# Kernel optimization log

Measured on AMD Instinct MI355X. Metric: run time of the kernel, lower is better.

Reference implementation:

```python
import jax, jax.numpy as jnp
import numpy as np

H = 64          # rnn_hidden_dim
HYP = 64        # api_hyper_dim
N_AG = 8
N_EN = 8
N_AL = 7
E_FEAT = 9
A_FEAT = 10
OWN_FEAT = 16
N_ACT = 14


def setup_inputs() -> dict:
    key = jax.random.key(0)
    ks = jax.random.split(key, 24)
    bs = 4096
    inp = {
        "own_feats": jax.random.normal(ks[0], (bs * N_AG, OWN_FEAT), jnp.float32),
        "enemy_feats": jax.random.normal(ks[1], (bs * N_AG * N_EN, E_FEAT), jnp.float32),
        "ally_feats": jax.random.normal(ks[2], (bs * N_AG * N_AL, A_FEAT), jnp.float32),
        "hidden_state": jax.random.normal(ks[3], (bs * N_AG, H), jnp.float32),
        "agent_indices": jax.random.randint(ks[4], (bs * N_AG,), 0, N_AG),
        "last_action_indices": jax.random.randint(ks[5], (bs * N_AG,), 0, N_ACT),
        "bs": bs,
    }
    s = 0.05
    inp.update({
        "fc1_own_w": jax.random.normal(ks[6], (OWN_FEAT, H), jnp.float32) * s,
        "fc1_own_b": jnp.zeros((H,), jnp.float32),
        "agent_id_emb": jax.random.normal(ks[7], (N_AG, H), jnp.float32) * s,
        "action_id_emb": jax.random.normal(ks[8], (N_ACT, H), jnp.float32) * s,
        "he_w1": jax.random.normal(ks[9], (E_FEAT, HYP), jnp.float32) * s,
        "he_b1": jnp.zeros((HYP,), jnp.float32),
        "he_w2": jax.random.normal(ks[10], (HYP, (E_FEAT + 1) * H + 1), jnp.float32) * s,
        "he_b2": jnp.zeros(((E_FEAT + 1) * H + 1,), jnp.float32),
        "ha_w1": jax.random.normal(ks[11], (A_FEAT, HYP), jnp.float32) * s,
        "ha_b1": jnp.zeros((HYP,), jnp.float32),
        "ha_w2": jax.random.normal(ks[12], (HYP, A_FEAT * H), jnp.float32) * s,
        "ha_b2": jnp.zeros((A_FEAT * H,), jnp.float32),
        "gru_w_ih": jax.random.normal(ks[13], (3 * H, H), jnp.float32) * s,
        "gru_w_hh": jax.random.normal(ks[14], (3 * H, H), jnp.float32) * s,
        "gru_b_ih": jnp.zeros((3 * H,), jnp.float32),
        "gru_b_hh": jnp.zeros((3 * H,), jnp.float32),
        "fc2_w": jax.random.normal(ks[15], (H, 6), jnp.float32) * s,
        "fc2_b": jnp.zeros((6,), jnp.float32),
    })
    return inp


def reference(own_feats, enemy_feats, ally_feats, hidden_state,
              fc1_own_w, fc1_own_b, agent_id_emb, action_id_emb,
              he_w1, he_b1, he_w2, he_b2, ha_w1, ha_b1, ha_w2, ha_b2,
              gru_w_ih, gru_w_hh, gru_b_ih, gru_b_hh, fc2_w, fc2_b,
              agent_indices, last_action_indices, bs):
    # own embedding + id/action embeddings  [bs*n_ag, H]
    emb_own = own_feats @ fc1_own_w + fc1_own_b
    emb_own = emb_own + agent_id_emb[agent_indices] + action_id_emb[last_action_indices]

    # enemy hypernet: [bs*n_ag*n_en, (E_FEAT+1)*H + 1]
    hyper_e = jax.nn.relu(enemy_feats @ he_w1 + he_b1) @ he_w2 + he_b2
    fc1_w_e = hyper_e[:, :-(H + 1)].reshape(-1, E_FEAT, H)
    emb_en = jnp.einsum('ne,neh->nh', enemy_feats, fc1_w_e)
    emb_en = emb_en.reshape(bs * N_AG, N_EN, H).sum(axis=1)

    # ally hypernet (non-MMM): [bs*n_ag*n_al, A_FEAT*H]
    hyper_a = jax.nn.relu(ally_feats @ ha_w1 + ha_b1) @ ha_w2 + ha_b2
    fc1_w_a = hyper_a.reshape(-1, A_FEAT, H)
    emb_al = jnp.einsum('na,nah->nh', ally_feats, fc1_w_a)
    emb_al = emb_al.reshape(bs * N_AG, N_AL, H).sum(axis=1)

    x = jax.nn.relu(emb_own + emb_en + emb_al)

    # torch GRUCell
    h_in = hidden_state.reshape(-1, H)
    gi = x @ gru_w_ih.T + gru_b_ih
    gh = h_in @ gru_w_hh.T + gru_b_hh
    i_r, i_z, i_n = jnp.split(gi, 3, axis=-1)
    h_r, h_z, h_n = jnp.split(gh, 3, axis=-1)
    r = jax.nn.sigmoid(i_r + h_r)
    z = jax.nn.sigmoid(i_z + h_z)
    n = jnp.tanh(i_n + r * h_n)
    hh = (1.0 - z) * n + z * h_in

    q_normal = (hh @ fc2_w + fc2_b).reshape(bs, N_AG, 6)

    # attack head from enemy hypernet tail
    fc2_w_attack = hyper_e[:, -(H + 1):-1].reshape(bs * N_AG, N_EN, H)
    fc2_b_attack = hyper_e[:, -1].reshape(bs * N_AG, N_EN)
    q_attack = (jnp.einsum('nh,neh->ne', hh, fc2_w_attack) + fc2_b_attack).reshape(bs, N_AG, N_EN)

    q = jnp.concatenate([q_normal, q_attack], axis=-1)
    return q.reshape(bs, N_AG, -1), hh.reshape(bs, N_AG, H)
```

## Files before the change

kernel.cpp:

```cpp
#include <hip/hip_runtime.h>
#include <hip/hip_bf16.h>

typedef short short8 __attribute__((ext_vector_type(8)));
typedef float f32x4 __attribute__((ext_vector_type(4)));

#define HD 64
#define N_EN 8
#define N_AL 7
#define E_FEAT 9
#define A_FEAT 10
#define OWN_FEAT 16
#define N_ACT 14
#define EW2 641
#define AW2 640

#define KSE 20
#define KSA 21
#define KSG 5
#define KSU 3

#define BE_OFF 0
#define BE_CNT (KSE*4*64*8)
#define BA_OFF (BE_OFF+BE_CNT)
#define BA_CNT (KSA*4*64*8)
#define BG_OFF (BA_OFF+BA_CNT)
#define BG_CNT (KSG*16*64*8)
#define BU_OFF (BG_OFF+BG_CNT)
#define BU_CNT (KSU*5*64*8)
#define WS_SHORTS (BU_OFF+BU_CNT)

#define P_STRIDE 676
#define LDS_AG 0
#define LDS_GATES 8192
#define LDS_AU 17024
#define LDS_U 0
#define LDS_BYTES 21632

__device__ __forceinline__ ushort f2u(float x) {
    __hip_bfloat16 b = __float2bfloat16(x);
    ushort u; __builtin_memcpy(&u, &b, 2); return u;
}
__device__ __forceinline__ float u2f(uint u) {
    union { uint x; float f; } c; c.x = u << 16; return c.f;
}
__device__ __forceinline__ uint pk2(float a, float b) {
    return (uint)f2u(a) | ((uint)f2u(b) << 16);
}
__device__ __forceinline__ float sigm(float x) { return 1.f / (1.f + __expf(-x)); }
__device__ __forceinline__ short8 lda(const char* base, int row, int strideB, int s, int g) {
    const char* p = base + row * strideB + s * 64 + g * 8;
    union { short8 v; uint2 q[2]; } u;
    u.q[0] = *(const uint2*)p;
    u.q[1] = *(const uint2*)(p + 32);
    return u.v;
}

__global__ __launch_bounds__(256) void prep_kernel(
    const float* __restrict__ he_w2, const float* __restrict__ he_b2,
    const float* __restrict__ ha_w2, const float* __restrict__ ha_b2,
    const float* __restrict__ fc1_own_w, const float* __restrict__ fc1_own_b,
    const float* __restrict__ agent_id_emb, const float* __restrict__ action_id_emb,
    const float* __restrict__ gru_w_ih, const float* __restrict__ gru_w_hh,
    const float* __restrict__ gru_b_ih, const float* __restrict__ gru_b_hh,
    const float* __restrict__ fc2_w, const float* __restrict__ fc2_b,
    ushort* __restrict__ ws)
{
    const int GE = KSE * 4, GA = KSA * 4, GG = KSG * 16, GU = KSU * 5;
    const int total = (GE + GA + GG + GU) * 64;
    int idx = blockIdx.x * 256 + threadIdx.x;
    if (idx >= total) return;
    int grp = idx >> 6, lane = idx & 63;
    int g = lane >> 4, col16 = lane & 15;
    int table, s, t, slot;
    if (grp < GE)           { table = 0; int q = grp;            s = q / 4;  t = q % 4;  slot = q * 64 + lane; }
    else if (grp < GE + GA) { table = 1; int q = grp - GE;       s = q / 4;  t = q % 4;  slot = q * 64 + lane; }
    else if (grp < GE + GA + GG) { table = 2; int q = grp - GE - GA; s = q / 16; t = q % 16; slot = q * 64 + lane; }
    else                    { table = 3; int q = grp - GE - GA - GG; s = q / 5; t = q % 5; slot = q * 64 + lane; }
    const int j = t * 16 + col16;
    ushort out[8];
    #pragma unroll
    for (int e = 0; e < 8; ++e) {
        int kk = 32 * s + 4 * g + (e & 3) + 16 * (e >> 2);
        float v = 0.f;
        if (table == 0) {
            if (kk < 576)      { int f = kk >> 6, k = kk & 63; v = he_w2[k * EW2 + f * HD + j]; }
            else if (kk < 585) { int f = kk - 576; v = he_b2[f * HD + j]; }
            else if (kk < 601) { int f = kk - 585; v = fc1_own_w[f * HD + j]; }
            else if (kk == 601){ v = fc1_own_b[j]; }
            else if (kk < 610) { int a = kk - 602; v = agent_id_emb[a * HD + j]; }
            else if (kk < 624) { int a = kk - 610; v = action_id_emb[a * HD + j]; }
        } else if (table == 1) {
            if (kk < 640)      { int f = kk >> 6, k = kk & 63; v = ha_w2[k * AW2 + f * HD + j]; }
            else if (kk < 650) { int f = kk - 640; v = ha_b2[f * HD + j]; }
        } else if (table == 2) {
            int gb = j >> 6, c = j & 63;
            if (gb <= 1) {
                int jj = gb * 64 + c;
                if (kk < 64)        v = gru_w_ih[jj * HD + kk];
                else if (kk < 128)  v = gru_w_hh[jj * HD + kk - 64];
                else if (kk == 128) v = gru_b_ih[jj] + gru_b_hh[jj];
            } else if (gb == 2) {
                int jj = 128 + c;
                if (kk < 64)        v = gru_w_ih[jj * HD + kk];
                else if (kk == 128) v = gru_b_ih[jj];
            } else {
                int jj = 128 + c;
                if (kk >= 64 && kk < 128) v = gru_w_hh[jj * HD + kk - 64];
                else if (kk == 128)       v = gru_b_hh[jj];
            }
        } else {
            if (j < 64) {
                if (kk < 64)       v = he_w2[j * EW2 + 576 + kk];
                else if (kk == 64) v = he_w2[j * EW2 + 640];
            } else if (j < 70) {
                int o = j - 64;
                if (kk < 64)       v = fc2_w[kk * 6 + o];
                else if (kk == 64) v = fc2_b[o];
            } else if (j == 70) {
                if (kk < 64)       v = he_b2[576 + kk];
                else if (kk == 64) v = he_b2[640];
            }
        }
        out[e] = f2u(v);
    }
    ushort* dst = ws + ((table == 0) ? BE_OFF : (table == 1) ? BA_OFF : (table == 2) ? BG_OFF : BU_OFF);
    *(short8*)(dst + slot * 8) = *(short8*)out;
}

__global__ __launch_bounds__(256, 2) void agent_kernel(
    const float* __restrict__ own_feats,
    const float* __restrict__ enemy_feats,
    const float* __restrict__ ally_feats,
    const float* __restrict__ hidden_state,
    const int*  __restrict__ agent_idx,
    const int*  __restrict__ last_act_idx,
    const float* __restrict__ he_w1, const float* __restrict__ he_b1,
    const float* __restrict__ ha_w1, const float* __restrict__ ha_b1,
    const ushort* __restrict__ ws,
    float* __restrict__ out_q, float* __restrict__ out_hh)
{
    __shared__ __align__(16) char smem[LDS_BYTES];
    const int tid  = threadIdx.x;
    const int lane = tid & 63;
    const int wv   = tid >> 6;
    const int n0   = blockIdx.x * 16;
    const int arow = lane & 15;
    const int g    = lane >> 4;
    ushort* P = (ushort*)smem;

    {
        float w1[E_FEAT];
        #pragma unroll
        for (int f = 0; f < E_FEAT; ++f) w1[f] = he_w1[f * HD + lane];
        const float b1 = he_b1[lane];
        #pragma unroll
        for (int rr = 0; rr < 4; ++rr) {
            const int row = wv * 4 + rr, n = n0 + row;
            const float* efb = enemy_feats + (size_t)n * (N_EN * E_FEAT);
            float pf[E_FEAT], sf[E_FEAT];
            #pragma unroll
            for (int f = 0; f < E_FEAT; ++f) { pf[f] = 0.f; sf[f] = 0.f; }
            #pragma unroll
            for (int e = 0; e < N_EN; ++e) {
                float ef[E_FEAT];
                #pragma unroll
                for (int f = 0; f < E_FEAT; ++f) ef[f] = efb[e * E_FEAT + f];
                float acc = b1;
                #pragma unroll
                for (int f = 0; f < E_FEAT; ++f) acc += ef[f] * w1[f];
                const float r = fmaxf(acc, 0.f);
                #pragma unroll
                for (int f = 0; f < E_FEAT; ++f) { pf[f] += r * ef[f]; sf[f] += ef[f]; }
            }
            ushort* Pr = P + row * P_STRIDE;
            #pragma unroll
            for (int f = 0; f < E_FEAT; ++f) Pr[f * HD + lane] = f2u(pf[f]);
            if (lane == 0) {
                #pragma unroll
                for (int f = 0; f < E_FEAT; ++f) Pr[576 + f] = f2u(sf[f]);
                Pr[601] = 0x3F80;
            }
            if (lane < OWN_FEAT) Pr[585 + lane] = f2u(own_feats[(size_t)n * OWN_FEAT + lane]);
            const int ai = agent_idx[n], la = last_act_idx[n];
            if (lane < 8)      Pr[602 + lane] = (lane == ai) ? 0x3F80 : 0;
            if (lane < N_ACT)  Pr[610 + lane] = (lane == la) ? 0x3F80 : 0;
            if (lane < 16)     Pr[624 + lane] = 0;
        }
    }
    __syncthreads();

    f32x4 accE = {0.f, 0.f, 0.f, 0.f};
    #pragma unroll
    for (int s = 0; s < KSE; ++s) {
        short8 b = *(const short8*)(ws + BE_OFF + ((size_t)(s * 4 + wv) * 64 + lane) * 8);
        short8 a = lda(smem, arow, P_STRIDE * 2, s, g);
        accE = __builtin_amdgcn_mfma_f32_16x16x32_bf16(a, b, accE, 0, 0, 0);
    }
    __syncthreads();

    {
        float w1[A_FEAT];
        #pragma unroll
        for (int f = 0; f < A_FEAT; ++f) w1[f] = ha_w1[f * HD + lane];
        const float b1 = ha_b1[lane];
        #pragma unroll
        for (int rr = 0; rr < 4; ++rr) {
            const int row = wv * 4 + rr, n = n0 + row;
            const float* afb = ally_feats + (size_t)n * (N_AL * A_FEAT);
            float pf[A_FEAT], sf[A_FEAT];
            #pragma unroll
            for (int f = 0; f < A_FEAT; ++f) { pf[f] = 0.f; sf[f] = 0.f; }
            #pragma unroll
            for (int e = 0; e < N_AL; ++e) {
                float af[A_FEAT];
                #pragma unroll
                for (int f = 0; f < A_FEAT; ++f) af[f] = afb[e * A_FEAT + f];
                float acc = b1;
                #pragma unroll
                for (int f = 0; f < A_FEAT; ++f) acc += af[f] * w1[f];
                const float r = fmaxf(acc, 0.f);
                #pragma unroll
                for (int f = 0; f < A_FEAT; ++f) { pf[f] += r * af[f]; sf[f] += af[f]; }
            }
            ushort* Pr = P + row * P_STRIDE;
            #pragma unroll
            for (int f = 0; f < A_FEAT; ++f) Pr[f * HD + lane] = f2u(pf[f]);
            if (lane == 0) {
                #pragma unroll
                for (int f = 0; f < A_FEAT; ++f) Pr[640 + f] = f2u(sf[f]);
            }
            if (lane < 22) Pr[650 + lane] = 0;
        }
    }
    __syncthreads();

    #pragma unroll
    for (int s = 0; s < KSA; ++s) {
        short8 b = *(const short8*)(ws + BA_OFF + ((size_t)(s * 4 + wv) * 64 + lane) * 8);
        short8 a = lda(smem, arow, P_STRIDE * 2, s, g);
        accE = __builtin_amdgcn_mfma_f32_16x16x32_bf16(a, b, accE, 0, 0, 0);
    }
    __syncthreads();

    float4 h4s;
    #pragma unroll
    for (int j = 0; j < 4; ++j) {
        const int m = g * 4 + j;
        *(ushort*)(smem + LDS_AG + m * 328 + (wv * 16 + arow) * 2) = f2u(fmaxf(accE[j], 0.f));
    }
    {
        const int row = tid >> 4, c4 = (tid & 15) * 4;
        h4s = *(const float4*)(hidden_state + (size_t)(n0 + row) * HD + c4);
        char* p = smem + LDS_AG + row * 328 + (64 + c4) * 2;
        *(uint*)p       = pk2(h4s.x, h4s.y);
        *(uint*)(p + 4) = pk2(h4s.z, h4s.w);
        if (tid < 16) *(ushort*)(smem + LDS_AG + tid * 328 + 128 * 2) = 0x3F80;
        for (int i = tid; i < 16 * 31; i += 256) {
            int r2 = i / 31, c = 129 + i % 31;
            *(ushort*)(smem + LDS_AG + r2 * 328 + c * 2) = 0;
        }
    }
    __syncthreads();

    {
        f32x4 accG[4] = {{0.f,0.f,0.f,0.f},{0.f,0.f,0.f,0.f},{0.f,0.f,0.f,0.f},{0.f,0.f,0.f,0.f}};
        #pragma unroll
        for (int s = 0; s < KSG; ++s) {
            short8 a = lda(smem + LDS_AG, arow, 328, s, g);
            #pragma unroll
            for (int tt = 0; tt < 4; ++tt) {
                const int t = wv * 4 + tt;
                short8 b = *(const short8*)(ws + BG_OFF + ((size_t)(s * 16 + t) * 64 + lane) * 8);
                accG[tt] = __builtin_amdgcn_mfma_f32_16x16x32_bf16(a, b, accG[tt], 0, 0, 0);
            }
        }
        #pragma unroll
        for (int tt = 0; tt < 4; ++tt)
            #pragma unroll
            for (int j = 0; j < 4; ++j) {
                const int m = g * 4 + j, jc = (wv * 4 + tt) * 16 + arow;
                *(ushort*)(smem + LDS_GATES + m * 520 + jc * 2) = f2u(accG[tt][j]);
            }
    }
    __syncthreads();

    {
        const int row = tid >> 4, c4 = (tid & 15) * 4;
        const char* gb = smem + LDS_GATES + row * 520;
        uint2 rv = *(const uint2*)(gb + c4 * 2);
        uint2 zv = *(const uint2*)(gb + 128 + c4 * 2);
        uint2 iv = *(const uint2*)(gb + 256 + c4 * 2);
        uint2 nv = *(const uint2*)(gb + 384 + c4 * 2);
        float hr[4] = {u2f(rv.x & 0xffffu), u2f(rv.x >> 16), u2f(rv.y & 0xffffu), u2f(rv.y >> 16)};
        float hz[4] = {u2f(zv.x & 0xffffu), u2f(zv.x >> 16), u2f(zv.y & 0xffffu), u2f(zv.y >> 16)};
        float hi[4] = {u2f(iv.x & 0xffffu), u2f(iv.x >> 16), u2f(iv.y & 0xffffu), u2f(iv.y >> 16)};
        float hn[4] = {u2f(nv.x & 0xffffu), u2f(nv.x >> 16), u2f(nv.y & 0xffffu), u2f(nv.y >> 16)};
        float hcur[4] = {h4s.x, h4s.y, h4s.z, h4s.w};
        float hh[4];
        #pragma unroll
        for (int cc = 0; cc < 4; ++cc) {
            const float r = sigm(hr[cc]);
            const float z = sigm(hz[cc]);
            const float nng = tanhf(hi[cc] + r * hn[cc]);
            hh[cc] = (1.f - z) * nng + z * hcur[cc];
        }
        *(float4*)(out_hh + (size_t)(n0 + row) * HD + c4) = make_float4(hh[0], hh[1], hh[2], hh[3]);
        char* p = smem + LDS_AU + row * 200 + c4 * 2;
        *(uint*)p       = pk2(hh[0], hh[1]);
        *(uint*)(p + 4) = pk2(hh[2], hh[3]);
        if (tid < 16) *(ushort*)(smem + LDS_AU + tid * 200 + 64 * 2) = 0x3F80;
        for (int i = tid; i < 16 * 31; i += 256) {
            int r2 = i / 31, c = 65 + i % 31;
            *(ushort*)(smem + LDS_AU + r2 * 200 + c * 2) = 0;
        }
    }
    __syncthreads();

    {
        f32x4 accU = {0.f, 0.f, 0.f, 0.f};
        f32x4 accQ = {0.f, 0.f, 0.f, 0.f};
        #pragma unroll
        for (int s = 0; s < KSU; ++s) {
            short8 a = lda(smem + LDS_AU, arow, 200, s, g);
            short8 b = *(const short8*)(ws + BU_OFF + ((size_t)(s * 5 + wv) * 64 + lane) * 8);
            accU = __builtin_amdgcn_mfma_f32_16x16x32_bf16(a, b, accU, 0, 0, 0);
            if (wv == 0) {
                short8 b2 = *(const short8*)(ws + BU_OFF + ((size_t)(s * 5 + 4) * 64 + lane) * 8);
                accQ = __builtin_amdgcn_mfma_f32_16x16x32_bf16(a, b2, accQ, 0, 0, 0);
            }
        }
        float* uld = (float*)(smem + LDS_U);
        #pragma unroll
        for (int j = 0; j < 4; ++j) {
            const int m = g * 4 + j;
            uld[m * 66 + wv * 16 + arow] = accU[j];
        }
        if (wv == 0) {
            #pragma unroll
            for (int j = 0; j < 4; ++j) {
                const int m = g * 4 + j;
                if (arow < 6)       out_q[(size_t)(n0 + m) * N_ACT + arow] = accQ[j];
                else if (arow == 6) uld[m * 66 + 64] = accQ[j];
            }
        }
    }
    __syncthreads();

    {
        float w1[E_FEAT];
        #pragma unroll
        for (int f = 0; f < E_FEAT; ++f) w1[f] = he_w1[f * HD + lane];
        const float b1 = he_b1[lane];
        const float* uld = (const float*)(smem + LDS_U);
        #pragma unroll
        for (int rr = 0; rr < 4; ++rr) {
            const int row = wv * 4 + rr, n = n0 + row;
            const float uk = uld[row * 66 + lane];
            const float ct = uld[row * 66 + 64];
            const float* efb = enemy_feats + (size_t)n * (N_EN * E_FEAT);
            float p[N_EN];
            #pragma unroll
            for (int e = 0; e < N_EN; ++e) {
                float acc = b1;
                #pragma unroll
                for (int f = 0; f < E_FEAT; ++f) acc += efb[e * E_FEAT + f] * w1[f];
                p[e] = fmaxf(acc, 0.f) * uk;
            }
            #pragma unroll
            for (int o = 1; o < 64; o <<= 1) {
                #pragma unroll
                for (int e = 0; e < N_EN; ++e) p[e] += __shfl_xor(p[e], o);
            }
            if (lane < N_EN) {
                float pv = p[0];
                #pragma unroll
                for (int e = 1; e < N_EN; ++e) if (lane == e) pv = p[e];
                out_q[(size_t)n * N_ACT + 6 + lane] = pv + ct;
            }
        }
    }
}

extern "C" void kernel_launch(void* const* d_in, const int* in_sizes, int n_in,
                              void* d_out, int out_size, void* d_ws, size_t ws_size,
                              hipStream_t stream) {
    const float* own_feats    = (const float*)d_in[0];
    const float* enemy_feats  = (const float*)d_in[1];
    const float* ally_feats   = (const float*)d_in[2];
    const float* hidden_state = (const float*)d_in[3];
    const int*  agent_idx     = (const int*)d_in[4];
    const int*  last_act      = (const int*)d_in[5];
    const float* fc1_own_w = (const float*)d_in[7];
    const float* fc1_own_b = (const float*)d_in[8];
    const float* agent_id_emb  = (const float*)d_in[9];
    const float* action_id_emb = (const float*)d_in[10];
    const float* he_w1 = (const float*)d_in[11];
    const float* he_b1 = (const float*)d_in[12];
    const float* he_w2 = (const float*)d_in[13];
    const float* he_b2 = (const float*)d_in[14];
    const float* ha_w1 = (const float*)d_in[15];
    const float* ha_b1 = (const float*)d_in[16];
    const float* ha_w2 = (const float*)d_in[17];
    const float* ha_b2 = (const float*)d_in[18];
    const float* gru_w_ih = (const float*)d_in[19];
    const float* gru_w_hh = (const float*)d_in[20];
    const float* gru_b_ih = (const float*)d_in[21];
    const float* gru_b_hh = (const float*)d_in[22];
    const float* fc2_w = (const float*)d_in[23];
    const float* fc2_b = (const float*)d_in[24];

    const int R = in_sizes[0] / OWN_FEAT;
    ushort* ws = (ushort*)d_ws;
    float* out_q  = (float*)d_out;
    float* out_hh = out_q + (size_t)R * N_ACT;

    prep_kernel<<<65, 256, 0, stream>>>(
        he_w2, he_b2, ha_w2, ha_b2, fc1_own_w, fc1_own_b,
        agent_id_emb, action_id_emb, gru_w_ih, gru_w_hh, gru_b_ih, gru_b_hh,
        fc2_w, fc2_b, ws);

    agent_kernel<<<R / 16, 256, 0, stream>>>(
        own_feats, enemy_feats, ally_feats, hidden_state, agent_idx, last_act,
        he_w1, he_b1, ha_w1, ha_b1, ws, out_q, out_hh);
}
```

Measured before the change: 111.0 us.

## Double-buffer two 16-row tiles per block to overlap P-building with MFMA

```diff
diff --git a/kernel.cpp b/kernel.cpp
--- a/kernel.cpp
+++ b/kernel.cpp
@@ -14,27 +14,21 @@
 #define EW2 641
 #define AW2 640
 
-#define KSE 20
-#define KSA 21
-#define KSG 5
-#define KSU 3
+#define PW 640
+#define HALF 20480
+#define AG_OFF 0
+#define AG_STR 264
+#define GATES_OFF 4352
+#define GT_STR 520
+#define AU_OFF 12672
+#define AU_STR 136
+#define U_OFF 14848
 
 #define BE_OFF 0
-#define BE_CNT (KSE*4*64*8)
-#define BA_OFF (BE_OFF+BE_CNT)
-#define BA_CNT (KSA*4*64*8)
-#define BG_OFF (BA_OFF+BA_CNT)
-#define BG_CNT (KSG*16*64*8)
-#define BU_OFF (BG_OFF+BG_CNT)
-#define BU_CNT (KSU*5*64*8)
-#define WS_SHORTS (BU_OFF+BU_CNT)
-
-#define P_STRIDE 676
-#define LDS_AG 0
-#define LDS_GATES 8192
-#define LDS_AU 17024
-#define LDS_U 0
-#define LDS_BYTES 21632
+#define BA_OFF 40960
+#define BG_OFF 81920
+#define BU_OFF 114688
+#define WS_US 119808
 
 __device__ __forceinline__ ushort f2u(float x) {
     __hip_bfloat16 b = __float2bfloat16(x);
@@ -47,7 +41,17 @@
     return (uint)f2u(a) | ((uint)f2u(b) << 16);
 }
 __device__ __forceinline__ float sigm(float x) { return 1.f / (1.f + __expf(-x)); }
-__device__ __forceinline__ short8 lda(const char* base, int row, int strideB, int s, int g) {
+
+__device__ __forceinline__ short8 lda_swz(const ushort* P_us, int row, int s, int g) {
+    const int mm = (row & 7) << 3;
+    const int o = s * 32 + g * 4;
+    const ushort* pr = P_us + row * PW;
+    union { short8 v; uint2 q[2]; } u;
+    u.q[0] = *(const uint2*)(pr + (o ^ mm));
+    u.q[1] = *(const uint2*)(pr + ((o + 16) ^ mm));
+    return u.v;
+}
+__device__ __forceinline__ short8 lda_lin(const char* base, int row, int strideB, int s, int g) {
     const char* p = base + row * strideB + s * 64 + g * 8;
     union { short8 v; uint2 q[2]; } u;
     u.q[0] = *(const uint2*)p;
@@ -63,68 +67,282 @@
     const float* __restrict__ gru_w_ih, const float* __restrict__ gru_w_hh,
     const float* __restrict__ gru_b_ih, const float* __restrict__ gru_b_hh,
     const float* __restrict__ fc2_w, const float* __restrict__ fc2_b,
-    ushort* __restrict__ ws)
-{
-    const int GE = KSE * 4, GA = KSA * 4, GG = KSG * 16, GU = KSU * 5;
-    const int total = (GE + GA + GG + GU) * 64;
+    ushort* __restrict__ ws, float* __restrict__ fbias)
+{
+    const int GE = 80, GA = 80, GG = 64, GU = 10;
+    const int TT = (GE + GA + GG + GU) * 64;
     int idx = blockIdx.x * 256 + threadIdx.x;
-    if (idx >= total) return;
-    int grp = idx >> 6, lane = idx & 63;
-    int g = lane >> 4, col16 = lane & 15;
-    int table, s, t, slot;
-    if (grp < GE)           { table = 0; int q = grp;            s = q / 4;  t = q % 4;  slot = q * 64 + lane; }
-    else if (grp < GE + GA) { table = 1; int q = grp - GE;       s = q / 4;  t = q % 4;  slot = q * 64 + lane; }
-    else if (grp < GE + GA + GG) { table = 2; int q = grp - GE - GA; s = q / 16; t = q % 16; slot = q * 64 + lane; }
-    else                    { table = 3; int q = grp - GE - GA - GG; s = q / 5; t = q % 5; slot = q * 64 + lane; }
-    const int j = t * 16 + col16;
-    ushort out[8];
-    #pragma unroll
-    for (int e = 0; e < 8; ++e) {
-        int kk = 32 * s + 4 * g + (e & 3) + 16 * (e >> 2);
-        float v = 0.f;
-        if (table == 0) {
-            if (kk < 576)      { int f = kk >> 6, k = kk & 63; v = he_w2[k * EW2 + f * HD + j]; }
-            else if (kk < 585) { int f = kk - 576; v = he_b2[f * HD + j]; }
-            else if (kk < 601) { int f = kk - 585; v = fc1_own_w[f * HD + j]; }
-            else if (kk == 601){ v = fc1_own_b[j]; }
-            else if (kk < 610) { int a = kk - 602; v = agent_id_emb[a * HD + j]; }
-            else if (kk < 624) { int a = kk - 610; v = action_id_emb[a * HD + j]; }
-        } else if (table == 1) {
-            if (kk < 640)      { int f = kk >> 6, k = kk & 63; v = ha_w2[k * AW2 + f * HD + j]; }
-            else if (kk < 650) { int f = kk - 640; v = ha_b2[f * HD + j]; }
-        } else if (table == 2) {
-            int gb = j >> 6, c = j & 63;
-            if (gb <= 1) {
-                int jj = gb * 64 + c;
-                if (kk < 64)        v = gru_w_ih[jj * HD + kk];
-                else if (kk < 128)  v = gru_w_hh[jj * HD + kk - 64];
-                else if (kk == 128) v = gru_b_ih[jj] + gru_b_hh[jj];
-            } else if (gb == 2) {
-                int jj = 128 + c;
-                if (kk < 64)        v = gru_w_ih[jj * HD + kk];
-                else if (kk == 128) v = gru_b_ih[jj];
+    if (idx < TT) {
+        int grp = idx >> 6, lane = idx & 63;
+        int g = lane >> 4, col16 = lane & 15;
+        int table, s, t, slot;
+        if (grp < GE)                { table = 0; int q = grp;                s = q / 4;  t = q % 4;  slot = q * 64 + lane; }
+        else if (grp < GE + GA)      { table = 1; int q = grp - GE;           s = q / 4;  t = q % 4;  slot = q * 64 + lane; }
+        else if (grp < GE + GA + GG) { table = 2; int q = grp - GE - GA;      s = q / 16; t = q % 16; slot = q * 64 + lane; }
+        else                         { table = 3; int q = grp - GE - GA - GG; s = q / 5;  t = q % 5;  slot = q * 64 + lane; }
+        const int j = t * 16 + col16;
+        ushort out[8];
+        #pragma unroll
+        for (int e = 0; e < 8; ++e) {
+            int kk = 32 * s + 4 * g + (e & 3) + 16 * (e >> 2);
+            float v = 0.f;
+            if (table == 0) {
+                if (kk < 576)       v = he_w2[(kk & 63) * EW2 + (kk >> 6) * HD + j];
+                else if (kk < 585)  v = he_b2[(kk - 576) * HD + j];
+                else if (kk < 601)  v = fc1_own_w[(kk - 585) * HD + j];
+                else if (kk == 601) v = fc1_own_b[j];
+                else if (kk < 610)  v = agent_id_emb[(kk - 602) * HD + j];
+                else if (kk < 624)  v = action_id_emb[(kk - 610) * HD + j];
+                else if (kk < 634)  v = ha_b2[(kk - 624) * HD + j];
+            } else if (table == 1) {
+                v = ha_w2[(kk & 63) * AW2 + (kk >> 6) * HD + j];
+            } else if (table == 2) {
+                int gb2 = j >> 6, c = j & 63;
+                int jj = (gb2 == 0) ? c : (gb2 == 1) ? 64 + c : 128 + c;
+                if (gb2 <= 1)      v = (kk < 64) ? gru_w_ih[jj * HD + kk] : gru_w_hh[jj * HD + kk - 64];
+                else if (gb2 == 2) v = (kk < 64) ? gru_w_ih[jj * HD + kk] : 0.f;
+                else               v = (kk >= 64) ? gru_w_hh[jj * HD + kk - 64] : 0.f;
             } else {
-                int jj = 128 + c;
-                if (kk >= 64 && kk < 128) v = gru_w_hh[jj * HD + kk - 64];
-                else if (kk == 128)       v = gru_b_hh[jj];
+                if (j < 64)       v = he_w2[j * EW2 + 576 + kk];
+                else if (j < 70)  v = fc2_w[kk * 6 + (j - 64)];
+                else if (j == 70) v = he_b2[576 + kk];
             }
-        } else {
-            if (j < 64) {
-                if (kk < 64)       v = he_w2[j * EW2 + 576 + kk];
-                else if (kk == 64) v = he_w2[j * EW2 + 640];
-            } else if (j < 70) {
-                int o = j - 64;
-                if (kk < 64)       v = fc2_w[kk * 6 + o];
-                else if (kk == 64) v = fc2_b[o];
-            } else if (j == 70) {
-                if (kk < 64)       v = he_b2[576 + kk];
-                else if (kk == 64) v = he_b2[640];
-            }
-        }
-        out[e] = f2u(v);
-    }
-    ushort* dst = ws + ((table == 0) ? BE_OFF : (table == 1) ? BA_OFF : (table == 2) ? BG_OFF : BU_OFF);
-    *(short8*)(dst + slot * 8) = *(short8*)out;
+            out[e] = f2u(v);
+        }
+        ushort* dst = ws + ((table == 0) ? BE_OFF : (table == 1) ? BA_OFF : (table == 2) ? BG_OFF : BU_OFF);
+        *(short8*)(dst + (size_t)slot * 8) = *(short8*)out;
+    } else {
+        int b = idx - TT;
+        if (b < 128)       fbias[b] = gru_b_ih[b] + gru_b_hh[b];
+        else if (b < 192)  fbias[b] = gru_b_ih[b];
+        else if (b < 256)  fbias[b] = gru_b_hh[b - 64];
+        else if (b < 320)  fbias[b] = he_w2[(size_t)(b - 256) * EW2 + 640];
+        else if (b < 326)  fbias[b] = fc2_b[b - 320];
+        else if (b == 326) fbias[256 + 70] = he_b2[640];
+    }
+}
+
+__device__ __forceinline__ void pbuild_ally_row(
+    ushort* P_us, const float* __restrict__ ally_feats,
+    const float* w1, float b1, int n, int row, int lane)
+{
+    const int mm = (row & 7) << 3;
+    ushort* Pr = P_us + row * PW;
+    const float* afb = ally_feats + (size_t)n * (N_AL * A_FEAT);
+    float pf[A_FEAT];
+    #pragma unroll
+    for (int f = 0; f < A_FEAT; ++f) pf[f] = 0.f;
+    #pragma unroll
+    for (int e = 0; e < N_AL; ++e) {
+        float af[A_FEAT];
+        #pragma unroll
+        for (int f = 0; f < A_FEAT; ++f) af[f] = afb[e * A_FEAT + f];
+        float acc = b1;
+        #pragma unroll
+        for (int f = 0; f < A_FEAT; ++f) acc += af[f] * w1[f];
+        const float r = fmaxf(acc, 0.f);
+        #pragma unroll
+        for (int f = 0; f < A_FEAT; ++f) pf[f] += r * af[f];
+    }
+    #pragma unroll
+    for (int f = 0; f < A_FEAT; ++f) Pr[(f * HD + lane) ^ mm] = f2u(pf[f]);
+}
+
+__device__ __forceinline__ void pbuild_enemy_row(
+    ushort* P_us,
+    const float* __restrict__ enemy_feats, const float* __restrict__ ally_feats,
+    const float* __restrict__ own_feats,
+    const int* __restrict__ agent_idx, const int* __restrict__ last_act_idx,
+    const float* w1, float b1, int n, int row, int lane)
+{
+    const int mm = (row & 7) << 3;
+    ushort* Pr = P_us + row * PW;
+    const float* efb = enemy_feats + (size_t)n * (N_EN * E_FEAT);
+    float pf[E_FEAT];
+    #pragma unroll
+    for (int f = 0; f < E_FEAT; ++f) pf[f] = 0.f;
+    #pragma unroll
+    for (int e = 0; e < N_EN; ++e) {
+        float ef[E_FEAT];
+        #pragma unroll
+        for (int f = 0; f < E_FEAT; ++f) ef[f] = efb[e * E_FEAT + f];
+        float acc = b1;
+        #pragma unroll
+        for (int f = 0; f < E_FEAT; ++f) acc += ef[f] * w1[f];
+        const float r = fmaxf(acc, 0.f);
+        #pragma unroll
+        for (int f = 0; f < E_FEAT; ++f) pf[f] += r * ef[f];
+    }
+    #pragma unroll
+    for (int f = 0; f < E_FEAT; ++f) Pr[(f * HD + lane) ^ mm] = f2u(pf[f]);
+    if (lane < E_FEAT) {
+        float sv = 0.f;
+        #pragma unroll
+        for (int e = 0; e < N_EN; ++e) sv += efb[e * E_FEAT + lane];
+        Pr[(576 + lane) ^ mm] = f2u(sv);
+    }
+    if (lane < OWN_FEAT) Pr[(585 + lane) ^ mm] = f2u(own_feats[(size_t)n * OWN_FEAT + lane]);
+    if (lane == 0) Pr[601 ^ mm] = 0x3F80;
+    const int ai = agent_idx[n], la = last_act_idx[n];
+    if (lane < 8)     Pr[(602 + lane) ^ mm] = (lane == ai) ? (ushort)0x3F80 : (ushort)0;
+    if (lane < N_ACT) Pr[(610 + lane) ^ mm] = (lane == la) ? (ushort)0x3F80 : (ushort)0;
+    if (lane < A_FEAT) {
+        const float* afb = ally_feats + (size_t)n * (N_AL * A_FEAT);
+        float sv = 0.f;
+        #pragma unroll
+        for (int e = 0; e < N_AL; ++e) sv += afb[e * A_FEAT + lane];
+        Pr[(624 + lane) ^ mm] = f2u(sv);
+    }
+}
+
+__device__ __forceinline__ void gemm5(f32x4& acc, const ushort* P_us, const ushort* bt,
+                                      int rr, int wv, int lane, int arow, int g)
+{
+    #pragma unroll
+    for (int s5 = 0; s5 < 5; ++s5) {
+        const int s = rr * 5 + s5;
+        short8 b = *(const short8*)(bt + ((size_t)(s * 4 + wv) * 64 + lane) * 8);
+        short8 a = lda_swz(P_us, arow, s, g);
+        acc = __builtin_amdgcn_mfma_f32_16x16x32_bf16(a, b, acc, 0, 0, 0);
+    }
+}
+
+__device__ __forceinline__ void stageAG(char* H, const f32x4& acc,
+    const float* __restrict__ hidden_state, int n0g, int tid, int wv, int arow, int g)
+{
+    char* AGb = H + AG_OFF;
+    #pragma unroll
+    for (int j = 0; j < 4; ++j)
+        *(ushort*)(AGb + (g * 4 + j) * AG_STR + (wv * 16 + arow) * 2) = f2u(fmaxf(acc[j], 0.f));
+    const int row = tid >> 4, c4 = (tid & 15) * 4;
+    float4 h4 = *(const float4*)(hidden_state + (size_t)(n0g + row) * HD + c4);
+    char* p = AGb + row * AG_STR + (64 + c4) * 2;
+    *(uint*)p       = pk2(h4.x, h4.y);
+    *(uint*)(p + 4) = pk2(h4.z, h4.w);
+}
+
+__device__ __forceinline__ void gru_gemm(char* H, const ushort* __restrict__ ws,
+                                         int wv, int lane, int arow, int g)
+{
+    f32x4 accG[4] = {{0.f,0.f,0.f,0.f},{0.f,0.f,0.f,0.f},{0.f,0.f,0.f,0.f},{0.f,0.f,0.f,0.f}};
+    #pragma unroll
+    for (int s = 0; s < 4; ++s) {
+        short8 a = lda_lin(H + AG_OFF, arow, AG_STR, s, g);
+        #pragma unroll
+        for (int tt = 0; tt < 4; ++tt) {
+            const int t = wv * 4 + tt;
+            short8 b = *(const short8*)(ws + BG_OFF + ((size_t)(s * 16 + t) * 64 + lane) * 8);
+            accG[tt] = __builtin_amdgcn_mfma_f32_16x16x32_bf16(a, b, accG[tt], 0, 0, 0);
+        }
+    }
+    #pragma unroll
+    for (int tt = 0; tt < 4; ++tt)
+        #pragma unroll
+        for (int j = 0; j < 4; ++j)
+            *(ushort*)(H + GATES_OFF + (g * 4 + j) * GT_STR + ((wv * 4 + tt) * 16 + arow) * 2) = f2u(accG[tt][j]);
+}
+
+__device__ __forceinline__ void pointwise(char* H, const float* __restrict__ hidden_state,
+    const float* __restrict__ fbias, float* __restrict__ out_hh, int n0g, int tid)
+{
+    const int row = tid >> 4, c4 = (tid & 15) * 4;
+    const char* gb = H + GATES_OFF + row * GT_STR;
+    uint2 rv = *(const uint2*)(gb + c4 * 2);
+    uint2 zv = *(const uint2*)(gb + 128 + c4 * 2);
+    uint2 iv = *(const uint2*)(gb + 256 + c4 * 2);
+    uint2 nv = *(const uint2*)(gb + 384 + c4 * 2);
+    float4 bR = *(const float4*)(fbias + c4);
+    float4 bZ = *(const float4*)(fbias + 64 + c4);
+    float4 bI = *(const float4*)(fbias + 128 + c4);
+    float4 bH = *(const float4*)(fbias + 192 + c4);
+    float4 h4 = *(const float4*)(hidden_state + (size_t)(n0g + row) * HD + c4);
+    float gr[4] = {u2f(rv.x & 0xffffu) + bR.x, u2f(rv.x >> 16) + bR.y, u2f(rv.y & 0xffffu) + bR.z, u2f(rv.y >> 16) + bR.w};
+    float gz[4] = {u2f(zv.x & 0xffffu) + bZ.x, u2f(zv.x >> 16) + bZ.y, u2f(zv.y & 0xffffu) + bZ.z, u2f(zv.y >> 16) + bZ.w};
+    float gi[4] = {u2f(iv.x & 0xffffu) + bI.x, u2f(iv.x >> 16) + bI.y, u2f(iv.y & 0xffffu) + bI.z, u2f(iv.y >> 16) + bI.w};
+    float gn[4] = {u2f(nv.x & 0xffffu) + bH.x, u2f(nv.x >> 16) + bH.y, u2f(nv.y & 0xffffu) + bH.z, u2f(nv.y >> 16) + bH.w};
+    float hcur[4] = {h4.x, h4.y, h4.z, h4.w};
+    float hh[4];
+    #pragma unroll
+    for (int cc = 0; cc < 4; ++cc) {
+        const float r = sigm(gr[cc]);
+        const float z = sigm(gz[cc]);
+        const float nng = tanhf(gi[cc] + r * gn[cc]);
+        hh[cc] = (1.f - z) * nng + z * hcur[cc];
+    }
+    *(float4*)(out_hh + (size_t)(n0g + row) * HD + c4) = make_float4(hh[0], hh[1], hh[2], hh[3]);
+    char* p = H + AU_OFF + row * AU_STR + c4 * 2;
+    *(uint*)p       = pk2(hh[0], hh[1]);
+    *(uint*)(p + 4) = pk2(hh[2], hh[3]);
+}
+
+__device__ __forceinline__ void u_gemm(char* H, const ushort* __restrict__ ws,
+    const float* __restrict__ fbias, float* __restrict__ out_q,
+    int n0g, int wv, int lane, int arow, int g)
+{
+    f32x4 accU = {0.f, 0.f, 0.f, 0.f};
+    f32x4 accQ = {0.f, 0.f, 0.f, 0.f};
+    #pragma unroll
+    for (int s = 0; s < 2; ++s) {
+        short8 a = lda_lin(H + AU_OFF, arow, AU_STR, s, g);
+        short8 b = *(const short8*)(ws + BU_OFF + ((size_t)(s * 5 + wv) * 64 + lane) * 8);
+        accU = __builtin_amdgcn_mfma_f32_16x16x32_bf16(a, b, accU, 0, 0, 0);
+        if (wv == 0) {
+            short8 b2 = *(const short8*)(ws + BU_OFF + ((size_t)(s * 5 + 4) * 64 + lane) * 8);
+            accQ = __builtin_amdgcn_mfma_f32_16x16x32_bf16(a, b2, accQ, 0, 0, 0);
+        }
+    }
+    float* uld = (float*)(H + U_OFF);
+    #pragma unroll
+    for (int j = 0; j < 4; ++j)
+        uld[(g * 4 + j) * 66 + wv * 16 + arow] = accU[j];
+    if (wv == 0) {
+        #pragma unroll
+        for (int j = 0; j < 4; ++j) {
+            const int m = g * 4 + j;
+            if (arow < 6)       out_q[(size_t)(n0g + m) * N_ACT + arow] = accQ[j] + fbias[320 + arow];
+            else if (arow == 6) uld[m * 66 + 64] = accQ[j];
+        }
+    }
+}
+
+__device__ __forceinline__ void attack(char* H, const float* __restrict__ enemy_feats,
+    const float* __restrict__ he_w1, const float* __restrict__ he_b1,
+    const float* __restrict__ fbias, float* __restrict__ out_q,
+    int n0g, int wv, int lane)
+{
+    float w1[E_FEAT];
+    #pragma unroll
+    for (int f = 0; f < E_FEAT; ++f) w1[f] = he_w1[f * HD + lane];
+    const float b1 = he_b1[lane];
+    const float ubl = fbias[256 + lane];
+    const float cb = fbias[256 + 70];
+    const float* uld = (const float*)(H + U_OFF);
+    #pragma unroll
+    for (int rr = 0; rr < 4; ++rr) {
+        const int row = wv * 4 + rr, n = n0g + row;
+        const float uk = uld[row * 66 + lane] + ubl;
+        const float ct = uld[row * 66 + 64] + cb;
+        const float* efb = enemy_feats + (size_t)n * (N_EN * E_FEAT);
+        float p[N_EN];
+        #pragma unroll
+        for (int e = 0; e < N_EN; ++e) {
+            float acc = b1;
+            #pragma unroll
+            for (int f = 0; f < E_FEAT; ++f) acc += efb[e * E_FEAT + f] * w1[f];
+            p[e] = fmaxf(acc, 0.f) * uk;
+        }
+        #pragma unroll
+        for (int o = 1; o < 64; o <<= 1) {
+            #pragma unroll
+            for (int e = 0; e < N_EN; ++e) p[e] += __shfl_xor(p[e], o);
+        }
+        if (lane < N_EN) {
+            float pv = p[0];
+            #pragma unroll
+            for (int e = 1; e < N_EN; ++e) if (lane == e) pv = p[e];
+            out_q[(size_t)n * N_ACT + 6 + lane] = pv + ct;
+        }
+    }
 }
 
 __global__ __launch_bounds__(256, 2) void agent_kernel(
@@ -136,18 +354,42 @@
     const int*  __restrict__ last_act_idx,
     const float* __restrict__ he_w1, const float* __restrict__ he_b1,
     const float* __restrict__ ha_w1, const float* __restrict__ ha_b1,
-    const ushort* __restrict__ ws,
+    const ushort* __restrict__ ws, const float* __restrict__ fbias,
     float* __restrict__ out_q, float* __restrict__ out_hh)
 {
-    __shared__ __align__(16) char smem[LDS_BYTES];
-    const int tid  = threadIdx.x;
-    const int lane = tid & 63;
-    const int wv   = tid >> 6;
-    const int n0   = blockIdx.x * 16;
-    const int arow = lane & 15;
-    const int g    = lane >> 4;
-    ushort* P = (ushort*)smem;
-
+    __shared__ __align__(16) char smem[2 * HALF];
+    const int tid = threadIdx.x, lane = tid & 63, wv = tid >> 6;
+    const int arow = lane & 15, g = lane >> 4;
+    const int n0A = blockIdx.x * 32, n0B = n0A + 16;
+    ushort* PA = (ushort*)smem;
+    ushort* PB = (ushort*)(smem + HALF);
+    char* HA = smem;
+    char* HB = smem + HALF;
+
+    f32x4 accA = {0.f, 0.f, 0.f, 0.f}, accB = {0.f, 0.f, 0.f, 0.f};
+
+    {
+        float w1[A_FEAT];
+        #pragma unroll
+        for (int f = 0; f < A_FEAT; ++f) w1[f] = ha_w1[f * HD + lane];
+        const float b1 = ha_b1[lane];
+        #pragma unroll
+        for (int rr = 0; rr < 4; ++rr)
+            pbuild_ally_row(PA, ally_feats, w1, b1, n0A + wv * 4 + rr, wv * 4 + rr, lane);
+    }
+    __syncthreads();
+    {
+        float w1[A_FEAT];
+        #pragma unroll
+        for (int f = 0; f < A_FEAT; ++f) w1[f] = ha_w1[f * HD + lane];
+        const float b1 = ha_b1[lane];
+        #pragma unroll
+        for (int rr = 0; rr < 4; ++rr) {
+            gemm5(accA, PA, ws + BA_OFF, rr, wv, lane, arow, g);
+            pbuild_ally_row(PB, ally_feats, w1, b1, n0B + wv * 4 + rr, wv * 4 + rr, lane);
+        }
+    }
+    __syncthreads();
     {
         float w1[E_FEAT];
         #pragma unroll
@@ -155,230 +397,53 @@
         const float b1 = he_b1[lane];
         #pragma unroll
         for (int rr = 0; rr < 4; ++rr) {
-            const int row = wv * 4 + rr, n = n0 + row;
-            const float* efb = enemy_feats + (size_t)n * (N_EN * E_FEAT);
-            float pf[E_FEAT], sf[E_FEAT];
-            #pragma unroll
-            for (int f = 0; f < E_FEAT; ++f) { pf[f] = 0.f; sf[f] = 0.f; }
-            #pragma unroll
-            for (int e = 0; e < N_EN; ++e) {
-                float ef[E_FEAT];
-                #pragma unroll
-                for (int f = 0; f < E_FEAT; ++f) ef[f] = efb[e * E_FEAT + f];
-                float acc = b1;
-                #pragma unroll
-                for (int f = 0; f < E_FEAT; ++f) acc += ef[f] * w1[f];
-                const float r = fmaxf(acc, 0.f);
-                #pragma unroll
-                for (int f = 0; f < E_FEAT; ++f) { pf[f] += r * ef[f]; sf[f] += ef[f]; }
-            }
-            ushort* Pr = P + row * P_STRIDE;
-            #pragma unroll
-            for (int f = 0; f < E_FEAT; ++f) Pr[f * HD + lane] = f2u(pf[f]);
-            if (lane == 0) {
-                #pragma unroll
-                for (int f = 0; f < E_FEAT; ++f) Pr[576 + f] = f2u(sf[f]);
-                Pr[601] = 0x3F80;
-            }
-            if (lane < OWN_FEAT) Pr[585 + lane] = f2u(own_feats[(size_t)n * OWN_FEAT + lane]);
-            const int ai = agent_idx[n], la = last_act_idx[n];
-            if (lane < 8)      Pr[602 + lane] = (lane == ai) ? 0x3F80 : 0;
-            if (lane < N_ACT)  Pr[610 + lane] = (lane == la) ? 0x3F80 : 0;
-            if (lane < 16)     Pr[624 + lane] = 0;
-        }
-    }
-    __syncthreads();
-
-    f32x4 accE = {0.f, 0.f, 0.f, 0.f};
-    #pragma unroll
-    for (int s = 0; s < KSE; ++s) {
-        short8 b = *(const short8*)(ws + BE_OFF + ((size_t)(s * 4 + wv) * 64 + lane) * 8);
-        short8 a = lda(smem, arow, P_STRIDE * 2, s, g);
-        accE = __builtin_amdgcn_mfma_f32_16x16x32_bf16(a, b, accE, 0, 0, 0);
-    }
-    __syncthreads();
-
-    {
-        float w1[A_FEAT];
-        #pragma unroll
-        for (int f = 0; f < A_FEAT; ++f) w1[f] = ha_w1[f * HD + lane];
-        const float b1 = ha_b1[lane];
-        #pragma unroll
-        for (int rr = 0; rr < 4; ++rr) {
-            const int row = wv * 4 + rr, n = n0 + row;
-            const float* afb = ally_feats + (size_t)n * (N_AL * A_FEAT);
-            float pf[A_FEAT], sf[A_FEAT];
-            #pragma unroll
-            for (int f = 0; f < A_FEAT; ++f) { pf[f] = 0.f; sf[f] = 0.f; }
-            #pragma unroll
-            for (int e = 0; e < N_AL; ++e) {
-                float af[A_FEAT];
-                #pragma unroll
-                for (int f = 0; f < A_FEAT; ++f) af[f] = afb[e * A_FEAT + f];
-                float acc = b1;
-                #pragma unroll
-                for (int f = 0; f < A_FEAT; ++f) acc += af[f] * w1[f];
-                const float r = fmaxf(acc, 0.f);
-                #pragma unroll
-                for (int f = 0; f < A_FEAT; ++f) { pf[f] += r * af[f]; sf[f] += af[f]; }
-            }
-            ushort* Pr = P + row * P_STRIDE;
-            #pragma unroll
-            for (int f = 0; f < A_FEAT; ++f) Pr[f * HD + lane] = f2u(pf[f]);
-            if (lane == 0) {
-                #pragma unroll
-                for (int f = 0; f < A_FEAT; ++f) Pr[640 + f] = f2u(sf[f]);
-            }
-            if (lane < 22) Pr[650 + lane] = 0;
-        }
-    }
-    __syncthreads();
-
-    #pragma unroll
-    for (int s = 0; s < KSA; ++s) {
-        short8 b = *(const short8*)(ws + BA_OFF + ((size_t)(s * 4 + wv) * 64 + lane) * 8);
-        short8 a = lda(smem, arow, P_STRIDE * 2, s, g);
-        accE = __builtin_amdgcn_mfma_f32_16x16x32_bf16(a, b, accE, 0, 0, 0);
-    }
-    __syncthreads();
-
-    float4 h4s;
-    #pragma unroll
-    for (int j = 0; j < 4; ++j) {
-        const int m = g * 4 + j;
-        *(ushort*)(smem + LDS_AG + m * 328 + (wv * 16 + arow) * 2) = f2u(fmaxf(accE[j], 0.f));
-    }
-    {
-        const int row = tid >> 4, c4 = (tid & 15) * 4;
-        h4s = *(const float4*)(hidden_state + (size_t)(n0 + row) * HD + c4);
-        char* p = smem + LDS_AG + row * 328 + (64 + c4) * 2;
-        *(uint*)p       = pk2(h4s.x, h4s.y);
-        *(uint*)(p + 4) = pk2(h4s.z, h4s.w);
-        if (tid < 16) *(ushort*)(smem + LDS_AG + tid * 328 + 128 * 2) = 0x3F80;
-        for (int i = tid; i < 16 * 31; i += 256) {
-            int r2 = i / 31, c = 129 + i % 31;
-            *(ushort*)(smem + LDS_AG + r2 * 328 + c * 2) = 0;
-        }
-    }
-    __syncthreads();
-
-    {
-        f32x4 accG[4] = {{0.f,0.f,0.f,0.f},{0.f,0.f,0.f,0.f},{0.f,0.f,0.f,0.f},{0.f,0.f,0.f,0.f}};
-        #pragma unroll
-        for (int s = 0; s < KSG; ++s) {
-            short8 a = lda(smem + LDS_AG, arow, 328, s, g);
-            #pragma unroll
-            for (int tt = 0; tt < 4; ++tt) {
-                const int t = wv * 4 + tt;
-                short8 b = *(const short8*)(ws + BG_OFF + ((size_t)(s * 16 + t) * 64 + lane) * 8);
-                accG[tt] = __builtin_amdgcn_mfma_f32_16x16x32_bf16(a, b, accG[tt], 0, 0, 0);
-            }
-        }
-        #pragma unroll
-        for (int tt = 0; tt < 4; ++tt)
-            #pragma unroll
-            for (int j = 0; j < 4; ++j) {
-                const int m = g * 4 + j, jc = (wv * 4 + tt) * 16 + arow;
-                *(ushort*)(smem + LDS_GATES + m * 520 + jc * 2) = f2u(accG[tt][j]);
-            }
-    }
-    __syncthreads();
-
-    {
-        const int row = tid >> 4, c4 = (tid & 15) * 4;
-        const char* gb = smem + LDS_GATES + row * 520;
-        uint2 rv = *(const uint2*)(gb + c4 * 2);
-        uint2 zv = *(const uint2*)(gb + 128 + c4 * 2);
-        uint2 iv = *(const uint2*)(gb + 256 + c4 * 2);
-        uint2 nv = *(const uint2*)(gb + 384 + c4 * 2);
-        float hr[4] = {u2f(rv.x & 0xffffu), u2f(rv.x >> 16), u2f(rv.y & 0xffffu), u2f(rv.y >> 16)};
-        float hz[4] = {u2f(zv.x & 0xffffu), u2f(zv.x >> 16), u2f(zv.y & 0xffffu), u2f(zv.y >> 16)};
-        float hi[4] = {u2f(iv.x & 0xffffu), u2f(iv.x >> 16), u2f(iv.y & 0xffffu), u2f(iv.y >> 16)};
-        float hn[4] = {u2f(nv.x & 0xffffu), u2f(nv.x >> 16), u2f(nv.y & 0xffffu), u2f(nv.y >> 16)};
-        float hcur[4] = {h4s.x, h4s.y, h4s.z, h4s.w};
-        float hh[4];
-        #pragma unroll
-        for (int cc = 0; cc < 4; ++cc) {
-            const float r = sigm(hr[cc]);
-            const float z = sigm(hz[cc]);
-            const float nng = tanhf(hi[cc] + r * hn[cc]);
-            hh[cc] = (1.f - z) * nng + z * hcur[cc];
-        }
-        *(float4*)(out_hh + (size_t)(n0 + row) * HD + c4) = make_float4(hh[0], hh[1], hh[2], hh[3]);
-        char* p = smem + LDS_AU + row * 200 + c4 * 2;
-        *(uint*)p       = pk2(hh[0], hh[1]);
-        *(uint*)(p + 4) = pk2(hh[2], hh[3]);
-        if (tid < 16) *(ushort*)(smem + LDS_AU + tid * 200 + 64 * 2) = 0x3F80;
-        for (int i = tid; i < 16 * 31; i += 256) {
-            int r2 = i / 31, c = 65 + i % 31;
-            *(ushort*)(smem + LDS_AU + r2 * 200 + c * 2) = 0;
-        }
-    }
-    __syncthreads();
-
-    {
-        f32x4 accU = {0.f, 0.f, 0.f, 0.f};
-        f32x4 accQ = {0.f, 0.f, 0.f, 0.f};
-        #pragma unroll
-        for (int s = 0; s < KSU; ++s) {
-            short8 a = lda(smem + LDS_AU, arow, 200, s, g);
-            short8 b = *(const short8*)(ws + BU_OFF + ((size_t)(s * 5 + wv) * 64 + lane) * 8);
-            accU = __builtin_amdgcn_mfma_f32_16x16x32_bf16(a, b, accU, 0, 0, 0);
-            if (wv == 0) {
-                short8 b2 = *(const short8*)(ws + BU_OFF + ((size_t)(s * 5 + 4) * 64 + lane) * 8);
-                accQ = __builtin_amdgcn_mfma_f32_16x16x32_bf16(a, b2, accQ, 0, 0, 0);
-            }
-        }
-        float* uld = (float*)(smem + LDS_U);
-        #pragma unroll
-        for (int j = 0; j < 4; ++j) {
-            const int m = g * 4 + j;
-            uld[m * 66 + wv * 16 + arow] = accU[j];
-        }
-        if (wv == 0) {
-            #pragma unroll
-            for (int j = 0; j < 4; ++j) {
-                const int m = g * 4 + j;
-                if (arow < 6)       out_q[(size_t)(n0 + m) * N_ACT + arow] = accQ[j];
-                else if (arow == 6) uld[m * 66 + 64] = accQ[j];
-            }
-        }
-    }
-    __syncthreads();
-
+            gemm5(accB, PB, ws + BA_OFF, rr, wv, lane, arow, g);
+            pbuild_enemy_row(PA, enemy_feats, ally_feats, own_feats, agent_idx, last_act_idx,
+                             w1, b1, n0A + wv * 4 + rr, wv * 4 + rr, lane);
+        }
+    }
+    __syncthreads();
     {
         float w1[E_FEAT];
         #pragma unroll
         for (int f = 0; f < E_FEAT; ++f) w1[f] = he_w1[f * HD + lane];
         const float b1 = he_b1[lane];
-        const float* uld = (const float*)(smem + LDS_U);
         #pragma unroll
         for (int rr = 0; rr < 4; ++rr) {
-            const int row = wv * 4 + rr, n = n0 + row;
-            const float uk = uld[row * 66 + lane];
-            const float ct = uld[row * 66 + 64];
-            const float* efb = enemy_feats + (size_t)n * (N_EN * E_FEAT);
-            float p[N_EN];
-            #pragma unroll
-            for (int e = 0; e < N_EN; ++e) {
-                float acc = b1;
-                #pragma unroll
-                for (int f = 0; f < E_FEAT; ++f) acc += efb[e * E_FEAT + f] * w1[f];
-                p[e] = fmaxf(acc, 0.f) * uk;
-            }
-            #pragma unroll
-            for (int o = 1; o < 64; o <<= 1) {
-                #pragma unroll
-                for (int e = 0; e < N_EN; ++e) p[e] += __shfl_xor(p[e], o);
-            }
-            if (lane < N_EN) {
-                float pv = p[0];
-                #pragma unroll
-                for (int e = 1; e < N_EN; ++e) if (lane == e) pv = p[e];
-                out_q[(size_t)n * N_ACT + 6 + lane] = pv + ct;
-            }
-        }
-    }
+            gemm5(accA, PA, ws + BE_OFF, rr, wv, lane, arow, g);
+            pbuild_enemy_row(PB, enemy_feats, ally_feats, own_feats, agent_idx, last_act_idx,
+                             w1, b1, n0B + wv * 4 + rr, wv * 4 + rr, lane);
+        }
+    }
+    __syncthreads();
+    {
+        #pragma unroll
+        for (int rr = 0; rr < 4; ++rr)
+            gemm5(accB, PB, ws + BE_OFF, rr, wv, lane, arow, g);
+        stageAG(HA, accA, hidden_state, n0A, tid, wv, arow, g);
+    }
+    __syncthreads();
+    {
+        gru_gemm(HA, ws, wv, lane, arow, g);
+        stageAG(HB, accB, hidden_state, n0B, tid, wv, arow, g);
+    }
+    __syncthreads();
+    {
+        gru_gemm(HB, ws, wv, lane, arow, g);
+        pointwise(HA, hidden_state, fbias, out_hh, n0A, tid);
+    }
+    __syncthreads();
+    {
+        u_gemm(HA, ws, fbias, out_q, n0A, wv, lane, arow, g);
+        pointwise(HB, hidden_state, fbias, out_hh, n0B, tid);
+    }
+    __syncthreads();
+    {
+        u_gemm(HB, ws, fbias, out_q, n0B, wv, lane, arow, g);
+        attack(HA, enemy_feats, he_w1, he_b1, fbias, out_q, n0A, wv, lane);
+    }
+    __syncthreads();
+    attack(HB, enemy_feats, he_w1, he_b1, fbias, out_q, n0B, wv, lane);
 }
 
 extern "C" void kernel_launch(void* const* d_in, const int* in_sizes, int n_in,
@@ -411,15 +476,16 @@
 
     const int R = in_sizes[0] / OWN_FEAT;
     ushort* ws = (ushort*)d_ws;
+    float* fbias = (float*)(ws + WS_US);
     float* out_q  = (float*)d_out;
     float* out_hh = out_q + (size_t)R * N_ACT;
 
-    prep_kernel<<<65, 256, 0, stream>>>(
+    prep_kernel<<<60, 256, 0, stream>>>(
         he_w2, he_b2, ha_w2, ha_b2, fc1_own_w, fc1_own_b,
         agent_id_emb, action_id_emb, gru_w_ih, gru_w_hh, gru_b_ih, gru_b_hh,
-        fc2_w, fc2_b, ws);
-
-    agent_kernel<<<R / 16, 256, 0, stream>>>(
+        fc2_w, fc2_b, ws, fbias);
+
+    agent_kernel<<<R / 32, 256, 0, stream>>>(
         own_feats, enemy_feats, ally_feats, hidden_state, agent_idx, last_act,
-        he_w1, he_b1, ha_w1, ha_b1, ws, out_q, out_hh);
-}
+        he_w1, he_b1, ha_w1, ha_b1, ws, fbias, out_q, out_hh);
+}
```

Result: no change. 110.2 us (-0.7%).
